# Optimization experiments

Hardware: AMD Instinct MI355X
Metric: run time of the kernel (lower is better)

The kernel has to match this reference:

```python
import jax, jax.numpy as jnp
import numpy as np

N = 4096
TAU = 0.2          # args.tau relaxation temperature
EPS = 1e-10        # numerical guard for logit of clamped probs


def setup_inputs() -> dict:
    key = jax.random.key(0)
    k1, k2, k3 = jax.random.split(key, 3)
    r = jax.random.uniform(k1, (N, N))
    ori_adj = jnp.where(r < 0.005, -1.0, jnp.where(r < 0.01, 1.0, 0.0)).astype(jnp.float32)
    # nn.init.uniform_(change_links_prob, 0.0, 0.001)
    change_links_prob = jax.random.uniform(k2, (N, N), minval=0.0, maxval=0.001, dtype=jnp.float32)
    # uniform noise for the RelaxedBernoulli logistic reparameterization
    u = jax.random.uniform(k3, (N, N), minval=1e-6, maxval=1.0 - 1e-6, dtype=jnp.float32)
    return {"ori_adj": ori_adj, "change_links_prob": change_links_prob, "u": u}


def reference(ori_adj, change_links_prob, u):
    # --- get_modified_adj: RelaxedBernoulliStraightThrough(tau, clamp(p,0,1)).rsample() ---
    p = jnp.clip(change_links_prob, EPS, 1.0 - EPS)      # torch.clamp(p, 0, 1) + logit guard
    logits = jnp.log(p) - jnp.log1p(-p)
    noise = jnp.log(u) - jnp.log1p(-u)                   # logistic noise
    soft = jax.nn.sigmoid((logits + noise) / TAU)        # relaxed sample
    hard = jnp.round(soft)                               # quantized sample
    change_prob = soft + jax.lax.stop_gradient(hard - soft)  # straight-through
    mod_adj = ori_adj + change_prob * (-2.0 * ori_adj)   # ori_adj * (1 - 2*b)

    # --- balance_degree_directed(mod_adj) ---
    # torch.diag(matrix) returns the diagonal VECTOR, broadcast-subtracted per row (faithful).
    A = mod_adj + mod_adj.T - jnp.diag(mod_adj)
    A_abs = jnp.abs(A)
    tr3 = jnp.einsum('ij,jk,ki->', A, A, A)              # trace(A @ A @ A)
    tr3_abs = jnp.einsum('ij,jk,ki->', A_abs, A_abs, A_abs)
    balance = 0.5 * (1.0 + tr3 / tr3_abs)
    return mod_adj, balance
```

## Files before the change

kernel.cpp:

```cpp
#include <hip/hip_runtime.h>
#include <hip/hip_bf16.h>
#include <cstdint>
#include <cstddef>

#define N 4096
#define NN ((size_t)N * (size_t)N)

typedef int   int4v   __attribute__((ext_vector_type(4)));
typedef float float4v __attribute__((ext_vector_type(4)));

__device__ inline void async16(const void* g, void* lds) {
    __builtin_amdgcn_global_load_lds(
        (const __attribute__((address_space(1))) void*)g,
        (__attribute__((address_space(3))) void*)lds, 16, 0, 0);
}

__global__ void fused_mod_build(const float* __restrict__ ori,
                                const float* __restrict__ clp,
                                const float* __restrict__ uu,
                                float* __restrict__ out,
                                signed char* __restrict__ A,
                                signed char* __restrict__ AT,
                                signed char* __restrict__ Aa,
                                signed char* __restrict__ ATa,
                                double* __restrict__ accs) {
    const int I = blockIdx.x, J = blockIdx.y;
    if (I > J) return;
    __shared__ float sm1[32][33];
    __shared__ float sm2[32][33];
    __shared__ float dI[32], dJ[32];
    const int tx = threadIdx.x;
    const int ty = threadIdx.y;
    const int t = ty * 8 + tx;
    const int bi = I * 32, bj = J * 32;
    if (I == 0 && J == 0 && t < 2) accs[t] = 0.0;
    if (t < 64) {
        const int x = (t < 32) ? (bi + t) : (bj + (t - 32));
        const size_t off = (size_t)x * N + x;
        const float o = ori[off];
        const float hard = (clp[off] + uu[off] >= 1.0f) ? 1.0f : 0.0f;
        const float d = fmaf(hard, -2.0f * o, o);
        if (t < 32) dI[t] = d; else dJ[t - 32] = d;
    }
    {
        const size_t off = (size_t)(bi + ty) * N + bj + tx * 4;
        const float4v o4 = *(const float4v*)(ori + off);
        const float4v p4 = *(const float4v*)(clp + off);
        const float4v u4 = *(const float4v*)(uu + off);
        float4v m;
        #pragma unroll
        for (int c = 0; c < 4; ++c) {
            const float hard = (p4[c] + u4[c] >= 1.0f) ? 1.0f : 0.0f;
            m[c] = fmaf(hard, -2.0f * o4[c], o4[c]);
            sm1[ty][tx * 4 + c] = m[c];
        }
        *(float4v*)(out + off) = m;
    }
    {
        const size_t off = (size_t)(bj + ty) * N + bi + tx * 4;
        const float4v o4 = *(const float4v*)(ori + off);
        const float4v p4 = *(const float4v*)(clp + off);
        const float4v u4 = *(const float4v*)(uu + off);
        float4v m;
        #pragma unroll
        for (int c = 0; c < 4; ++c) {
            const float hard = (p4[c] + u4[c] >= 1.0f) ? 1.0f : 0.0f;
            m[c] = fmaf(hard, -2.0f * o4[c], o4[c]);
            sm2[ty][tx * 4 + c] = m[c];
        }
        if (I != J) *(float4v*)(out + off) = m;
    }
    __syncthreads();
    int pkA1 = 0, pkAa1 = 0, pkT1 = 0, pkTa1 = 0;
    int pkA2 = 0, pkAa2 = 0, pkT2 = 0, pkTa2 = 0;
    #pragma unroll
    for (int k = 0; k < 4; ++k) {
        const int c = tx * 4 + k;
        const float a1 = sm1[ty][c] + sm2[c][ty] - dJ[c];
        const int v1 = (int)a1;  const int u1 = v1 < 0 ? -v1 : v1;
        pkA1  |= (v1 & 255) << (8 * k);
        pkAa1 |= (u1 & 255) << (8 * k);
        const float t1 = sm1[c][ty] + sm2[ty][c] - dJ[ty];
        const int w1 = (int)t1;  const int x1 = w1 < 0 ? -w1 : w1;
        pkT1  |= (w1 & 255) << (8 * k);
        pkTa1 |= (x1 & 255) << (8 * k);
        const float a2 = sm2[ty][c] + sm1[c][ty] - dI[c];
        const int v2 = (int)a2;  const int u2 = v2 < 0 ? -v2 : v2;
        pkA2  |= (v2 & 255) << (8 * k);
        pkAa2 |= (u2 & 255) << (8 * k);
        const float t2 = sm2[c][ty] + sm1[ty][c] - dI[ty];
        const int w2 = (int)t2;  const int x2 = w2 < 0 ? -w2 : w2;
        pkT2  |= (w2 & 255) << (8 * k);
        pkTa2 |= (x2 & 255) << (8 * k);
    }
    const size_t oIJ = (size_t)(bi + ty) * N + bj + tx * 4;
    const size_t oJI = (size_t)(bj + ty) * N + bi + tx * 4;
    *(int*)&A  [oIJ] = pkA1;
    *(int*)&Aa [oIJ] = pkAa1;
    *(int*)&AT [oJI] = pkT1;
    *(int*)&ATa[oJI] = pkTa1;
    if (I != J) {
        *(int*)&A  [oJI] = pkA2;
        *(int*)&Aa [oJI] = pkAa2;
        *(int*)&AT [oIJ] = pkT2;
        *(int*)&ATa[oIJ] = pkTa2;
    }
}

#define BK 64
#define NT (N / BK)
#define BUFSZ 32768

__global__ __launch_bounds__(512, 2) void gemm_trace_i8(
        const signed char* __restrict__ Ag,
        const signed char* __restrict__ ATg,
        const signed char* __restrict__ Aag,
        const signed char* __restrict__ ATag,
        double* __restrict__ accs) {
    __shared__ __align__(16) signed char lds[4 * BUFSZ];
    __shared__ int red[8];
    const int z = blockIdx.z;
    const signed char* Asrc = z ? Aag  : Ag;
    const signed char* Bsrc = z ? ATag : ATg;
    const int i0 = blockIdx.y * 256;
    const int k0 = blockIdx.x * 256;
    const int t = threadIdx.x;
    const int lane = t & 63;
    const int wave = t >> 6;
    const int wm = wave >> 2;
    const int wn = wave & 3;
    const int quad = lane >> 4;
    const int col  = lane & 15;

    const int c1 = t;
    const int r1 = c1 >> 2;
    const int r2 = r1 + 128;
    const int s1 = (((c1 & 3) ^ ((r1 >> 1) & 3)) << 4);
    const int s2 = (((c1 & 3) ^ ((r2 >> 1) & 3)) << 4);
    const signed char* gA1 = Asrc + (size_t)(i0 + r1) * N + s1;
    const signed char* gA2 = Asrc + (size_t)(i0 + r2) * N + s2;
    const signed char* gB1 = Bsrc + (size_t)(k0 + r1) * N + s1;
    const signed char* gB2 = Bsrc + (size_t)(k0 + r2) * N + s2;
    const int ldsA1 = (wave * 64) * 16;
    const int ldsA2 = 8192  + (wave * 64) * 16;
    const int ldsB1 = 16384 + (wave * 64) * 16;
    const int ldsB2 = 24576 + (wave * 64) * 16;
    const int fsw = ((quad ^ ((col >> 1) & 3)) << 4);

    int4v acc[8][4];
    #pragma unroll
    for (int a = 0; a < 8; ++a)
        #pragma unroll
        for (int b = 0; b < 4; ++b)
            acc[a][b] = (int4v){0, 0, 0, 0};

    for (int p = 0; p < 3; ++p) {
        const int pb = p * BUFSZ;
        const size_t go = (size_t)p * BK;
        async16(gA1 + go, lds + pb + ldsA1);
        async16(gA2 + go, lds + pb + ldsA2);
        async16(gB1 + go, lds + pb + ldsB1);
        async16(gB2 + go, lds + pb + ldsB2);
    }
    asm volatile("s_waitcnt vmcnt(8)" ::: "memory");
    __builtin_amdgcn_s_barrier();
    __builtin_amdgcn_sched_barrier(0);

    for (int j = 0; j < NT; ++j) {
        const int buf = (j & 3) * BUFSZ;
        const signed char* Ab = lds + buf;
        const signed char* Bb = lds + buf + 16384;
        const int pre = j + 3;
        const size_t go = (size_t)pre * BK;
        const int pb = (pre & 3) * BUFSZ;
        int4v af0[4], af1[4], bf[4];
        #pragma unroll
        for (int tr = 0; tr < 4; ++tr)
            af0[tr] = *(const int4v*)(Ab + ((wm * 128 + tr * 16 + col) << 6) + fsw);
        #pragma unroll
        for (int tc = 0; tc < 4; ++tc)
            bf[tc] = *(const int4v*)(Bb + ((wn * 64 + tc * 16 + col) << 6) + fsw);
        #pragma unroll
        for (int tr = 0; tr < 4; ++tr)
            af1[tr] = *(const int4v*)(Ab + ((wm * 128 + 64 + tr * 16 + col) << 6) + fsw);
        if (pre < NT) {
            async16(gA1 + go, lds + pb + ldsA1);
            async16(gA2 + go, lds + pb + ldsA2);
            async16(gB1 + go, lds + pb + ldsB1);
            async16(gB2 + go, lds + pb + ldsB2);
        }
        asm volatile("s_waitcnt lgkmcnt(4)" ::: "memory");
        __builtin_amdgcn_sched_barrier(0);
        __builtin_amdgcn_s_setprio(1);
        #pragma unroll
        for (int tr = 0; tr < 4; ++tr)
            #pragma unroll
            for (int tc = 0; tc < 4; ++tc)
                acc[tr][tc] = __builtin_amdgcn_mfma_i32_16x16x64_i8(af0[tr], bf[tc], acc[tr][tc], 0, 0, 0);
        __builtin_amdgcn_s_setprio(0);
        asm volatile("s_waitcnt lgkmcnt(0)" ::: "memory");
        __builtin_amdgcn_sched_barrier(0);
        __builtin_amdgcn_s_setprio(1);
        #pragma unroll
        for (int tr = 0; tr < 4; ++tr)
            #pragma unroll
            for (int tc = 0; tc < 4; ++tc)
                acc[4 + tr][tc] = __builtin_amdgcn_mfma_i32_16x16x64_i8(af1[tr], bf[tc], acc[4 + tr][tc], 0, 0, 0);
        __builtin_amdgcn_s_setprio(0);
        if (j < NT - 3)       { asm volatile("s_waitcnt vmcnt(8)" ::: "memory"); }
        else if (j == NT - 3) { asm volatile("s_waitcnt vmcnt(4)" ::: "memory"); }
        else if (j == NT - 2) { asm volatile("s_waitcnt vmcnt(0)" ::: "memory"); }
        __builtin_amdgcn_s_barrier();
        __builtin_amdgcn_sched_barrier(0);
    }

    int part = 0;
    #pragma unroll
    for (int mr = 0; mr < 8; ++mr) {
        const int ib = i0 + wm * 128 + mr * 16 + quad * 4;
        #pragma unroll
        for (int tc = 0; tc < 4; ++tc) {
            const int kk = k0 + wn * 64 + tc * 16 + col;
            const int mv = *(const int*)&Asrc[(size_t)kk * N + ib];
            #pragma unroll
            for (int r = 0; r < 4; ++r)
                part += acc[mr][tc][r] * (int)(signed char)(mv >> (8 * r));
        }
    }
    #pragma unroll
    for (int off = 32; off > 0; off >>= 1)
        part += __shfl_down(part, off, 64);
    if (lane == 0) red[wave] = part;
    __syncthreads();
    if (t == 0) {
        int tot = 0;
        #pragma unroll
        for (int w = 0; w < 8; ++w) tot += red[w];
        atomicAdd(&accs[z], (double)tot);
    }
}

__global__ void finalize_kernel(const double* __restrict__ accs, float* __restrict__ out) {
    out[NN] = (float)(0.5 * (1.0 + accs[0] / accs[1]));
}

extern "C" void kernel_launch(void* const* d_in, const int* in_sizes, int n_in,
                              void* d_out, int out_size, void* d_ws, size_t ws_size,
                              hipStream_t stream) {
    const float* ori = (const float*)d_in[0];
    const float* clp = (const float*)d_in[1];
    const float* u   = (const float*)d_in[2];
    float* out = (float*)d_out;
    char* ws = (char*)d_ws;
    signed char* A8   = (signed char*)ws;
    signed char* AT8  = (signed char*)(ws + NN);
    signed char* Aa8  = (signed char*)(ws + 2 * NN);
    signed char* ATa8 = (signed char*)(ws + 3 * NN);
    double*      accs = (double*)(ws + 4 * NN);

    fused_mod_build<<<dim3(128, 128), dim3(8, 32), 0, stream>>>(
        ori, clp, u, out, A8, AT8, Aa8, ATa8, accs);
    gemm_trace_i8<<<dim3(N / 256, N / 256, 2), 512, 0, stream>>>(A8, AT8, Aa8, ATa8, accs);
    finalize_kernel<<<1, 1, 0, stream>>>(accs, out);
}
```

Measured before the change: 381.0 us.

## Enlarge build tiles to 64x64 with 16B stores; finer-grained LDS waits in GEMM

The build kernel now uses 64x64 tiles with a 1D 256-thread block, so each thread writes packed int8 rows as 16-byte vector stores instead of 4-byte stores, which cuts store instruction count and launch/grid overhead. The GEMM inner loop reorders its LDS fragment loads and replaces two coarse lgkmcnt waits with per-row incremental waits, letting MFMAs start as soon as each A fragment arrives. The larger tile roughly doubles LDS per block in the build kernel and may lower its occupancy. The hand-counted waitcnt values must match the actual order in which the compiler issues the LDS loads.

```diff
diff --git a/kernel.cpp b/kernel.cpp
--- a/kernel.cpp
+++ b/kernel.cpp
@@ -15,35 +15,37 @@
         (__attribute__((address_space(3))) void*)lds, 16, 0, 0);
 }
 
-__global__ void fused_mod_build(const float* __restrict__ ori,
-                                const float* __restrict__ clp,
-                                const float* __restrict__ uu,
-                                float* __restrict__ out,
-                                signed char* __restrict__ A,
-                                signed char* __restrict__ AT,
-                                signed char* __restrict__ Aa,
-                                signed char* __restrict__ ATa,
-                                double* __restrict__ accs) {
+__global__ __launch_bounds__(256) void fused_mod_build(
+        const float* __restrict__ ori,
+        const float* __restrict__ clp,
+        const float* __restrict__ uu,
+        float* __restrict__ out,
+        signed char* __restrict__ A,
+        signed char* __restrict__ AT,
+        signed char* __restrict__ Aa,
+        signed char* __restrict__ ATa,
+        double* __restrict__ accs) {
     const int I = blockIdx.x, J = blockIdx.y;
     if (I > J) return;
-    __shared__ float sm1[32][33];
-    __shared__ float sm2[32][33];
-    __shared__ float dI[32], dJ[32];
-    const int tx = threadIdx.x;
-    const int ty = threadIdx.y;
-    const int t = ty * 8 + tx;
-    const int bi = I * 32, bj = J * 32;
+    __shared__ float sm1[64][65];
+    __shared__ float sm2[64][65];
+    __shared__ float dI[64], dJ[64];
+    const int t = threadIdx.x;
+    const int r = t >> 2;
+    const int q = t & 3;
+    const int bi = I * 64, bj = J * 64;
     if (I == 0 && J == 0 && t < 2) accs[t] = 0.0;
-    if (t < 64) {
-        const int x = (t < 32) ? (bi + t) : (bj + (t - 32));
+    if (t < 128) {
+        const int x = (t < 64) ? (bi + t) : (bj + (t - 64));
         const size_t off = (size_t)x * N + x;
         const float o = ori[off];
         const float hard = (clp[off] + uu[off] >= 1.0f) ? 1.0f : 0.0f;
         const float d = fmaf(hard, -2.0f * o, o);
-        if (t < 32) dI[t] = d; else dJ[t - 32] = d;
-    }
-    {
-        const size_t off = (size_t)(bi + ty) * N + bj + tx * 4;
+        if (t < 64) dI[t] = d; else dJ[t - 64] = d;
+    }
+    #pragma unroll
+    for (int k = 0; k < 4; ++k) {
+        const size_t off = (size_t)(bi + r) * N + bj + k * 16 + q * 4;
         const float4v o4 = *(const float4v*)(ori + off);
         const float4v p4 = *(const float4v*)(clp + off);
         const float4v u4 = *(const float4v*)(uu + off);
@@ -52,12 +54,13 @@
         for (int c = 0; c < 4; ++c) {
             const float hard = (p4[c] + u4[c] >= 1.0f) ? 1.0f : 0.0f;
             m[c] = fmaf(hard, -2.0f * o4[c], o4[c]);
-            sm1[ty][tx * 4 + c] = m[c];
+            sm1[r][k * 16 + q * 4 + c] = m[c];
         }
         *(float4v*)(out + off) = m;
     }
-    {
-        const size_t off = (size_t)(bj + ty) * N + bi + tx * 4;
+    #pragma unroll
+    for (int k = 0; k < 4; ++k) {
+        const size_t off = (size_t)(bj + r) * N + bi + k * 16 + q * 4;
         const float4v o4 = *(const float4v*)(ori + off);
         const float4v p4 = *(const float4v*)(clp + off);
         const float4v u4 = *(const float4v*)(uu + off);
@@ -66,44 +69,51 @@
         for (int c = 0; c < 4; ++c) {
             const float hard = (p4[c] + u4[c] >= 1.0f) ? 1.0f : 0.0f;
             m[c] = fmaf(hard, -2.0f * o4[c], o4[c]);
-            sm2[ty][tx * 4 + c] = m[c];
+            sm2[r][k * 16 + q * 4 + c] = m[c];
         }
         if (I != J) *(float4v*)(out + off) = m;
     }
     __syncthreads();
-    int pkA1 = 0, pkAa1 = 0, pkT1 = 0, pkTa1 = 0;
-    int pkA2 = 0, pkAa2 = 0, pkT2 = 0, pkTa2 = 0;
-    #pragma unroll
-    for (int k = 0; k < 4; ++k) {
-        const int c = tx * 4 + k;
-        const float a1 = sm1[ty][c] + sm2[c][ty] - dJ[c];
-        const int v1 = (int)a1;  const int u1 = v1 < 0 ? -v1 : v1;
-        pkA1  |= (v1 & 255) << (8 * k);
-        pkAa1 |= (u1 & 255) << (8 * k);
-        const float t1 = sm1[c][ty] + sm2[ty][c] - dJ[ty];
-        const int w1 = (int)t1;  const int x1 = w1 < 0 ? -w1 : w1;
-        pkT1  |= (w1 & 255) << (8 * k);
-        pkTa1 |= (x1 & 255) << (8 * k);
-        const float a2 = sm2[ty][c] + sm1[c][ty] - dI[c];
-        const int v2 = (int)a2;  const int u2 = v2 < 0 ? -v2 : v2;
-        pkA2  |= (v2 & 255) << (8 * k);
-        pkAa2 |= (u2 & 255) << (8 * k);
-        const float t2 = sm2[c][ty] + sm1[ty][c] - dI[ty];
-        const int w2 = (int)t2;  const int x2 = w2 < 0 ? -w2 : w2;
-        pkT2  |= (w2 & 255) << (8 * k);
-        pkTa2 |= (x2 & 255) << (8 * k);
-    }
-    const size_t oIJ = (size_t)(bi + ty) * N + bj + tx * 4;
-    const size_t oJI = (size_t)(bj + ty) * N + bi + tx * 4;
-    *(int*)&A  [oIJ] = pkA1;
-    *(int*)&Aa [oIJ] = pkAa1;
-    *(int*)&AT [oJI] = pkT1;
-    *(int*)&ATa[oJI] = pkTa1;
+    int pkA1[4], pkAa1[4], pkT1[4], pkTa1[4];
+    int pkA2[4], pkAa2[4], pkT2[4], pkTa2[4];
+    #pragma unroll
+    for (int w = 0; w < 4; ++w) {
+        int a1w = 0, aa1w = 0, t1w = 0, ta1w = 0;
+        int a2w = 0, aa2w = 0, t2w = 0, ta2w = 0;
+        #pragma unroll
+        for (int k = 0; k < 4; ++k) {
+            const int c = q * 16 + w * 4 + k;
+            const float a1 = sm1[r][c] + sm2[c][r] - dJ[c];
+            const int v1 = (int)a1;  const int u1 = v1 < 0 ? -v1 : v1;
+            a1w  |= (v1 & 255) << (8 * k);
+            aa1w |= (u1 & 255) << (8 * k);
+            const float t1 = sm1[c][r] + sm2[r][c] - dJ[r];
+            const int w1 = (int)t1;  const int x1 = w1 < 0 ? -w1 : w1;
+            t1w  |= (w1 & 255) << (8 * k);
+            ta1w |= (x1 & 255) << (8 * k);
+            const float a2 = sm2[r][c] + sm1[c][r] - dI[c];
+            const int v2 = (int)a2;  const int u2 = v2 < 0 ? -v2 : v2;
+            a2w  |= (v2 & 255) << (8 * k);
+            aa2w |= (u2 & 255) << (8 * k);
+            const float t2 = sm2[c][r] + sm1[r][c] - dI[r];
+            const int w2 = (int)t2;  const int x2 = w2 < 0 ? -w2 : w2;
+            t2w  |= (w2 & 255) << (8 * k);
+            ta2w |= (x2 & 255) << (8 * k);
+        }
+        pkA1[w] = a1w; pkAa1[w] = aa1w; pkT1[w] = t1w; pkTa1[w] = ta1w;
+        pkA2[w] = a2w; pkAa2[w] = aa2w; pkT2[w] = t2w; pkTa2[w] = ta2w;
+    }
+    const size_t oIJ = (size_t)(bi + r) * N + bj + q * 16;
+    const size_t oJI = (size_t)(bj + r) * N + bi + q * 16;
+    *(int4v*)&A  [oIJ] = *(int4v*)pkA1;
+    *(int4v*)&Aa [oIJ] = *(int4v*)pkAa1;
+    *(int4v*)&AT [oJI] = *(int4v*)pkT1;
+    *(int4v*)&ATa[oJI] = *(int4v*)pkTa1;
     if (I != J) {
-        *(int*)&A  [oJI] = pkA2;
-        *(int*)&Aa [oJI] = pkAa2;
-        *(int*)&AT [oIJ] = pkT2;
-        *(int*)&ATa[oIJ] = pkTa2;
+        *(int4v*)&A  [oJI] = *(int4v*)pkA2;
+        *(int4v*)&Aa [oJI] = *(int4v*)pkAa2;
+        *(int4v*)&AT [oIJ] = *(int4v*)pkT2;
+        *(int4v*)&ATa[oIJ] = *(int4v*)pkTa2;
     }
 }
 
@@ -174,12 +184,13 @@
         const size_t go = (size_t)pre * BK;
         const int pb = (pre & 3) * BUFSZ;
         int4v af0[4], af1[4], bf[4];
-        #pragma unroll
-        for (int tr = 0; tr < 4; ++tr)
-            af0[tr] = *(const int4v*)(Ab + ((wm * 128 + tr * 16 + col) << 6) + fsw);
+        af0[0] = *(const int4v*)(Ab + ((wm * 128 + 0 * 16 + col) << 6) + fsw);
         #pragma unroll
         for (int tc = 0; tc < 4; ++tc)
             bf[tc] = *(const int4v*)(Bb + ((wn * 64 + tc * 16 + col) << 6) + fsw);
+        #pragma unroll
+        for (int tr = 1; tr < 4; ++tr)
+            af0[tr] = *(const int4v*)(Ab + ((wm * 128 + tr * 16 + col) << 6) + fsw);
         #pragma unroll
         for (int tr = 0; tr < 4; ++tr)
             af1[tr] = *(const int4v*)(Ab + ((wm * 128 + 64 + tr * 16 + col) << 6) + fsw);
@@ -189,23 +200,33 @@
             async16(gB1 + go, lds + pb + ldsB1);
             async16(gB2 + go, lds + pb + ldsB2);
         }
-        asm volatile("s_waitcnt lgkmcnt(4)" ::: "memory");
+        __builtin_amdgcn_s_setprio(1);
+        asm volatile("s_waitcnt lgkmcnt(7)" ::: "memory");
         __builtin_amdgcn_sched_barrier(0);
-        __builtin_amdgcn_s_setprio(1);
-        #pragma unroll
-        for (int tr = 0; tr < 4; ++tr)
+        #pragma unroll
+        for (int tc = 0; tc < 4; ++tc)
+            acc[0][tc] = __builtin_amdgcn_mfma_i32_16x16x64_i8(af0[0], bf[tc], acc[0][tc], 0, 0, 0);
+        #pragma unroll
+        for (int tr = 1; tr < 4; ++tr) {
+            if (tr == 1)      asm volatile("s_waitcnt lgkmcnt(6)" ::: "memory");
+            else if (tr == 2) asm volatile("s_waitcnt lgkmcnt(5)" ::: "memory");
+            else              asm volatile("s_waitcnt lgkmcnt(4)" ::: "memory");
+            __builtin_amdgcn_sched_barrier(0);
             #pragma unroll
             for (int tc = 0; tc < 4; ++tc)
                 acc[tr][tc] = __builtin_amdgcn_mfma_i32_16x16x64_i8(af0[tr], bf[tc], acc[tr][tc], 0, 0, 0);
-        __builtin_amdgcn_s_setprio(0);
-        asm volatile("s_waitcnt lgkmcnt(0)" ::: "memory");
-        __builtin_amdgcn_sched_barrier(0);
-        __builtin_amdgcn_s_setprio(1);
-        #pragma unroll
-        for (int tr = 0; tr < 4; ++tr)
+        }
+        #pragma unroll
+        for (int tr = 0; tr < 4; ++tr) {
+            if (tr == 0)      asm volatile("s_waitcnt lgkmcnt(3)" ::: "memory");
+            else if (tr == 1) asm volatile("s_waitcnt lgkmcnt(2)" ::: "memory");
+            else if (tr == 2) asm volatile("s_waitcnt lgkmcnt(1)" ::: "memory");
+            else              asm volatile("s_waitcnt lgkmcnt(0)" ::: "memory");
+            __builtin_amdgcn_sched_barrier(0);
             #pragma unroll
             for (int tc = 0; tc < 4; ++tc)
                 acc[4 + tr][tc] = __builtin_amdgcn_mfma_i32_16x16x64_i8(af1[tr], bf[tc], acc[4 + tr][tc], 0, 0, 0);
+        }
         __builtin_amdgcn_s_setprio(0);
         if (j < NT - 3)       { asm volatile("s_waitcnt vmcnt(8)" ::: "memory"); }
         else if (j == NT - 3) { asm volatile("s_waitcnt vmcnt(4)" ::: "memory"); }
@@ -258,7 +279,7 @@
     signed char* ATa8 = (signed char*)(ws + 3 * NN);
     double*      accs = (double*)(ws + 4 * NN);
 
-    fused_mod_build<<<dim3(128, 128), dim3(8, 32), 0, stream>>>(
+    fused_mod_build<<<dim3(64, 64), 256, 0, stream>>>(
         ori, clp, u, out, A8, AT8, Aa8, ATa8, accs);
     gemm_trace_i8<<<dim3(N / 256, N / 256, 2), 512, 0, stream>>>(A8, AT8, Aa8, ATa8, accs);
     finalize_kernel<<<1, 1, 0, stream>>>(accs, out);
```

Measured after the change: 386.3 us. About the same (+1.4%).
